# Kernel tuning notes

Measured on AMD Instinct MI355X. Metric: run time of the kernel, lower is better.

The kernel has to match this reference:

```python
import jax, jax.numpy as jnp
import numpy as np

EPS = 1e-6

def setup_inputs() -> dict:
    key = jax.random.key(0)
    ks = jax.random.split(key, 12)
    B, C, H, W = 2, 192, 192, 192
    f = lambda k, s, sc=1.0: jax.random.normal(k, s, dtype=jnp.float32) * sc
    d = {}
    d["x_l"] = f(ks[0], (B, C, H, W))
    d["x_r"] = f(ks[1], (B, C, H, W))
    d["ln_l_w"] = jnp.ones((C,), jnp.float32)
    d["ln_l_b"] = jnp.zeros((C,), jnp.float32)
    d["ln_r_w"] = jnp.ones((C,), jnp.float32)
    d["ln_r_b"] = jnp.zeros((C,), jnp.float32)
    s = C ** -0.5
    d["wq_l"] = f(ks[2], (C, C), s)   # 1x1 conv weights as [out,in]
    d["wq_r"] = f(ks[3], (C, C), s)
    d["wv_l"] = f(ks[4], (C, C), s)
    d["wv_r"] = f(ks[5], (C, C), s)
    d["mlp_w1"] = f(ks[6], (C // 24, C // 3), (C // 3) ** -0.5)
    d["mlp_w2"] = f(ks[7], (C * 2 // 3, C // 24), (C // 24) ** -0.5)
    d["scale_h"] = jnp.ones((1,), jnp.float32)
    d["scale_w"] = jnp.ones((1,), jnp.float32)
    # layer scales are zero-init in the module; use small random so output is nontrivial
    d["ls1"] = f(ks[8], (1, C, 1, 1), 0.1)
    d["ls2"] = f(ks[9], (1, C, 1, 1), 0.1)
    return d

def _ln2d(x, w, b):
    # LayerNorm over channel dim of NCHW
    mu = x.mean(1, keepdims=True)
    var = ((x - mu) ** 2).mean(1, keepdims=True)
    return (x - mu) * jax.lax.rsqrt(var + EPS) * w[None, :, None, None] + b[None, :, None, None]

def _pw(x, w):
    # 1x1 conv, no bias
    return jnp.einsum('bchw,oc->bohw', x, w)

def reference(x_l, x_r, ln_l_w, ln_l_b, ln_r_w, ln_r_b, wq_l, wq_r, wv_l, wv_r,
              mlp_w1, mlp_w2, scale_h, scale_w, ls1, ls2):
    q_l_h, q_l_w, q_l_c = jnp.split(_pw(_ln2d(x_l, ln_l_w, ln_l_b), wq_l), 3, axis=1)
    q_r_h, q_r_w, q_r_c = jnp.split(_pw(_ln2d(x_r, ln_r_w, ln_r_b), wq_r), 3, axis=1)
    v_l_h, v_l_w, v_l_c = jnp.split(_pw(x_l, wv_l), 3, axis=1)
    v_r_h, v_r_w, v_r_c = jnp.split(_pw(x_r, wv_r), 3, axis=1)

    # height axial attention: scores [b, w, h, h']
    attn_h = jnp.einsum('bchw,bcgw->bwhg', q_l_h, q_r_h) * scale_h[0]
    attn_h = jax.nn.softmax(attn_h, axis=-1)
    x_r2l_h = jnp.einsum('bwhg,bcgw->bchw', attn_h, v_r_h)           # [b,c,h,w]
    x_l2r_h = jnp.einsum('bwhg,bchw->bcgw', attn_h, v_l_h)           # attn^T @ v_l

    # width axial attention: scores [b, h, w, w'] (softmax applied separately per direction)
    attn_w = jnp.einsum('bchw,bchv->bhwv', q_l_w, q_r_w) * scale_w[0]
    a1 = jax.nn.softmax(attn_w, axis=-1)
    x_r2l_w = jnp.einsum('bhwv,bchv->bchw', a1, v_r_w)
    a2 = jax.nn.softmax(jnp.swapaxes(attn_w, -1, -2), axis=-1)       # [b,h,v,w]
    x_l2r_w = jnp.einsum('bhvw,bchw->bchv', a2, v_l_w)

    # channel SE branch: sum of the two channel queries, GAP, bottleneck MLP
    p = (q_l_c + q_r_c).mean(axis=(2, 3))                            # [b, c]
    h1 = jax.nn.relu(p @ mlp_w1.T)                                   # [b, c//8]
    a = jax.nn.softmax(h1 @ mlp_w2.T, axis=1)                        # softmax over 2c channels jointly
    attn_l_c, attn_r_c = jnp.split(a, 2, axis=1)
    x_r2l_c = attn_l_c[:, :, None, None] * v_l_c
    x_l2r_c = attn_r_c[:, :, None, None] * v_r_c

    x_r2l = jnp.concatenate([x_r2l_h, x_r2l_w, x_r2l_c], axis=1)
    x_l2r = jnp.concatenate([x_l2r_h, x_l2r_w, x_l2r_c], axis=1)
    out_l = x_r2l * ls1 + x_l
    out_r = x_l2r * ls2 + x_r
    return (out_l, out_r)
```

## Files before the change

kernel.cpp:

```cpp
#include <hip/hip_runtime.h>
#include <stdint.h>

#define NN 36864
#define PL 7077888
#define PL64 2359296
#define TOT 14155776

typedef unsigned short ushort_t;
typedef __attribute__((ext_vector_type(8))) __bf16 bf16x8;
typedef __attribute__((ext_vector_type(4))) float f32x4;
typedef __attribute__((ext_vector_type(4))) unsigned int u32x4;
typedef __attribute__((ext_vector_type(2))) unsigned int u32x2;

__device__ __forceinline__ ushort_t f2bf(float f) {
  unsigned int u = __builtin_bit_cast(unsigned int, f);
  u = (u + 0x7FFFu + ((u >> 16) & 1u)) >> 16;
  return (ushort_t)u;
}
__device__ __forceinline__ float bf2f(ushort_t h) {
  unsigned int u = ((unsigned int)h) << 16;
  return __builtin_bit_cast(float, u);
}
__device__ __forceinline__ bf16x8 lds8(const ushort_t* p) {
  return __builtin_bit_cast(bf16x8, *(const u32x4*)p);
}
__device__ __forceinline__ f32x4 mfma16(bf16x8 a, bf16x8 b, f32x4 c) {
  return __builtin_amdgcn_mfma_f32_16x16x32_bf16(a, b, c, 0, 0, 0);
}
__device__ __forceinline__ unsigned cvtpk(float lo, float hi) {
  unsigned r;
  asm("v_cvt_pk_bf16_f32 %0, %1, %2" : "=v"(r) : "v"(lo), "v"(hi));
  return r;
}

__global__ void k_prep(const float* __restrict__ wq, const float* __restrict__ wv,
                       const float* __restrict__ lnw, const float* __restrict__ lnb,
                       ushort_t* __restrict__ W, float* __restrict__ ab) {
  __shared__ float sa[3], sb[3];
  int r = blockIdx.x, t = threadIdx.x;
  if (r < 192) {
    float w  = wq[r*192 + t];
    float lw = lnw[t], lb = lnb[t];
    W[r*192 + t] = f2bf(w * lw);
    float av = w * lb, bv = -w * lw;
    #pragma unroll
    for (int off = 1; off < 64; off <<= 1) {
      av += __shfl_xor(av, off);
      bv += __shfl_xor(bv, off);
    }
    if ((t & 63) == 0) { sa[t >> 6] = av; sb[t >> 6] = bv; }
    __syncthreads();
    if (t == 0) { ab[r] = sa[0]+sa[1]+sa[2]; ab[192 + r] = sb[0]+sb[1]+sb[2]; }
  } else {
    W[r*192 + t] = f2bf(wv[(r-192)*192 + t]);
  }
}

__global__ __launch_bounds__(512, 6) void k_proj(
    const float* __restrict__ xl, const float* __restrict__ xr,
    const ushort_t* __restrict__ Wl, const ushort_t* __restrict__ Wr,
    const float* __restrict__ abl, const float* __restrict__ abr,
    ushort_t* __restrict__ qhTl, ushort_t* __restrict__ qhTr,
    ushort_t* __restrict__ qwTl, ushort_t* __restrict__ qwTr,
    ushort_t* __restrict__ Vl, ushort_t* __restrict__ Vr,
    float* __restrict__ gpart) {
  __shared__ union {
    ushort_t B[64*192];
    ushort_t T[64*72];
  } sm;
  __shared__ float spart[8][64], spart2[8][64];
  __shared__ float smu[64], srs[64];
  __shared__ float gsum[64];

  const int bx = blockIdx.x;
  const int side = bx & 1;
  const int r0 = bx >> 1;
  const int ws = r0 % 3, bh = r0 / 3;
  const int b = bh / 192, h = bh % 192;
  const int w0 = ws * 64;

  const float*    x  = side ? xr  : xl;
  const ushort_t* W  = side ? Wr  : Wl;
  const float*    ab = side ? abr : abl;
  ushort_t* qhT = side ? qhTr : qhTl;
  ushort_t* qwT = side ? qwTr : qwTl;
  ushort_t* V   = side ? Vr   : Vl;

  const int tid = threadIdx.x;
  const int wave = tid >> 6, lane = tid & 63, lr = lane & 15, lg = lane >> 4;

  if (tid < 64) gsum[tid] = 0.f;

  {
    const int kq = wave, n = lane;
    const float* xb = x + (size_t)b*PL + h*192 + w0 + n;
    float gv[24];
    #pragma unroll
    for (int s = 0; s < 6; ++s)
      #pragma unroll
      for (int j = 0; j < 4; ++j)
        gv[s*4 + j] = xb[(size_t)(s*32 + kq*4 + j)*NN];
    float sA = 0.f, sB = 0.f;
    char* Bb = (char*)sm.B;
    const int slot = 16*((kq >> 1) ^ ((n >> 1) & 3)) + 8*(kq & 1);
    #pragma unroll
    for (int s = 0; s < 6; ++s) {
      union { ushort_t us[4]; u32x2 v; } t2;
      #pragma unroll
      for (int j = 0; j < 4; ++j) {
        float g = gv[s*4 + j];
        t2.us[j] = f2bf(g);
        sA += g; sB += g*g;
      }
      *(u32x2*)(Bb + n*384 + s*64 + slot) = t2.v;
    }
    spart[kq][n] = sA; spart2[kq][n] = sB;
  }
  __syncthreads();

  if (tid < 64) {
    float s = 0.f, s2 = 0.f;
    #pragma unroll
    for (int q = 0; q < 8; ++q) { s += spart[q][tid]; s2 += spart2[q][tid]; }
    float mu = s * (1.f/192.f);
    float var = s2 * (1.f/192.f) - mu*mu;
    smu[tid] = mu;
    srs[tid] = rsqrtf(var + 1e-6f);
  }

  const ushort_t* wbase = W + (size_t)(48*wave + lr)*192 + lg*8;
  const char* Bb = (const char*)sm.B;
  const f32x4 fz = {0.f, 0.f, 0.f, 0.f};
  f32x4 acc[3][4];
  #pragma unroll
  for (int mf = 0; mf < 3; ++mf)
    #pragma unroll
    for (int nf = 0; nf < 4; ++nf) acc[mf][nf] = fz;

  #pragma unroll
  for (int ks = 0; ks < 6; ++ks) {
    bf16x8 bfr[4];
    #pragma unroll
    for (int nf = 0; nf < 4; ++nf) {
      int n_ = nf*16 + lr;
      bfr[nf] = lds8((const ushort_t*)(Bb + n_*384 + ks*64 + 16*(lg ^ ((n_ >> 1) & 3))));
    }
    bf16x8 afr[3];
    #pragma unroll
    for (int mf = 0; mf < 3; ++mf)
      afr[mf] = lds8(wbase + (size_t)mf*16*192 + ks*32);
    #pragma unroll
    for (int mf = 0; mf < 3; ++mf)
      #pragma unroll
      for (int nf = 0; nf < 4; ++nf)
        acc[mf][nf] = mfma16(afr[mf], bfr[nf], acc[mf][nf]);
  }
  __syncthreads();

  if (wave < 4) {
    float rst[4], mrs[4];
    #pragma unroll
    for (int nf = 0; nf < 4; ++nf) {
      int n_ = nf*16 + lr;
      float rs = srs[n_];
      rst[nf] = rs;
      mrs[nf] = smu[n_] * rs;
    }
    #pragma unroll
    for (int mf = 0; mf < 3; ++mf) {
      int m = 48*wave + 16*mf + 4*lg;
      #pragma unroll
      for (int i = 0; i < 4; ++i) {
        float a_ = ab[m + i], bb = ab[192 + m + i];
        #pragma unroll
        for (int nf = 0; nf < 4; ++nf)
          acc[mf][nf][i] = acc[mf][nf][i]*rst[nf] + bb*mrs[nf] + a_;
      }
    }
  }

  char* Tb = (char*)sm.T;
  if (wave < 4) {
    #pragma unroll
    for (int mf = 0; mf < 3; ++mf) {
      int base = 48*wave + 16*mf;
      if ((base >> 6) == 0) {
        #pragma unroll
        for (int nf = 0; nf < 4; ++nf) {
          u32x2 v = { cvtpk(acc[mf][nf][0], acc[mf][nf][1]),
                      cvtpk(acc[mf][nf][2], acc[mf][nf][3]) };
          *(u32x2*)(Tb + (nf*16 + lr)*144 + (base + 4*lg)*2) = v;
        }
      }
    }
  }
  __syncthreads();
  {
    int w = tid >> 3, c8 = tid & 7;
    u32x4 v = *(const u32x4*)(Tb + w*144 + c8*16);
    *(u32x4*)&qhT[(((size_t)b*192 + w0 + w)*192 + h)*64 + c8*8] = v;
  }
  __syncthreads();

  if (wave < 4) {
    #pragma unroll
    for (int mf = 0; mf < 3; ++mf) {
      int base = 48*wave + 16*mf;
      if ((base >> 6) == 1) {
        #pragma unroll
        for (int nf = 0; nf < 4; ++nf) {
          u32x2 v = { cvtpk(acc[mf][nf][0], acc[mf][nf][1]),
                      cvtpk(acc[mf][nf][2], acc[mf][nf][3]) };
          *(u32x2*)(Tb + (nf*16 + lr)*144 + (base - 64 + 4*lg)*2) = v;
        }
      }
    }
  }
  __syncthreads();
  {
    int w = tid >> 3, c8 = tid & 7;
    u32x4 v = *(const u32x4*)(Tb + w*144 + c8*16);
    *(u32x4*)&qwT[(((size_t)b*192 + h)*192 + w0 + w)*64 + c8*8] = v;
  }
  __syncthreads();

  #pragma unroll
  for (int ch = 0; ch < 3; ++ch) {
    if (wave >= 4) {
      #pragma unroll
      for (int mf = 0; mf < 3; ++mf) {
        int vc = 48*(wave - 4) + 16*mf;
        if ((vc >> 6) == ch) {
          int cc = vc - 64*ch + 4*lg;
          #pragma unroll
          for (int nf = 0; nf < 4; ++nf)
            #pragma unroll
            for (int i = 0; i < 4; ++i)
              *(ushort_t*)(Tb + (cc + i)*144 + (nf*16 + lr)*2) = f2bf(acc[mf][nf][i]);
        }
      }
    } else if (ch == 0) {
      #pragma unroll
      for (int mf = 0; mf < 3; ++mf) {
        int base = 48*wave + 16*mf;
        if ((base >> 6) == 2) {
          #pragma unroll
          for (int i = 0; i < 4; ++i) {
            float part = acc[mf][0][i] + acc[mf][1][i] + acc[mf][2][i] + acc[mf][3][i];
            #pragma unroll
            for (int off = 1; off < 16; off <<= 1) part += __shfl_xor(part, off);
            if (lr == 0) atomicAdd(&gsum[base - 128 + 4*lg + i], part);
          }
        }
      }
    }
    __syncthreads();
    {
      int cc = tid >> 3, w8 = tid & 7;
      u32x4 v = *(const u32x4*)(Tb + cc*144 + w8*16);
      *(u32x4*)&V[((size_t)b*192 + ch*64 + cc)*NN + h*192 + w0 + w8*8] = v;
    }
    if (ch == 0 && tid < 64)
      gpart[(((size_t)(side*2 + b)*192 + h)*3 + ws)*64 + tid] = gsum[tid];
    __syncthreads();
  }
}

__global__ void k_repack_v(const ushort_t* __restrict__ Vl, const ushort_t* __restrict__ Vr,
                           ushort_t* __restrict__ vhTl, ushort_t* __restrict__ vhTr) {
  __shared__ ushort_t Ls[64*72];
  const ushort_t* V = blockIdx.y ? Vr : Vl;
  ushort_t* out = blockIdx.y ? vhTr : vhTl;
  int bx = blockIdx.x;
  int b = bx / 576, rem = bx % 576;
  int c = rem / 9, tt = rem % 9;
  int h0 = (tt/3)*64, w0 = (tt%3)*64;
  int tid = threadIdx.x;
  #pragma unroll
  for (int i = 0; i < 2; ++i) {
    int idx = tid + 256*i;
    int hh = idx >> 3, wb = idx & 7;
    *(u32x4*)&Ls[hh*72 + wb*8] =
      *(const u32x4*)&V[(size_t)(b*192 + c)*NN + (h0+hh)*192 + w0 + wb*8];
  }
  __syncthreads();
  #pragma unroll
  for (int i = 0; i < 2; ++i) {
    int idx = tid + 256*i;
    int ww = idx >> 3, hb = idx & 7;
    union { ushort_t us[8]; u32x4 v; } tu;
    #pragma unroll
    for (int j = 0; j < 8; ++j) tu.us[j] = Ls[(hb*8+j)*72 + ww];
    *(u32x4*)&out[(size_t)(b*64 + c)*NN + (w0+ww)*192 + h0 + hb*8] = tu.v;
  }
}

__global__ __launch_bounds__(256, 2) void k_attn(
    const ushort_t* __restrict__ qhTl, const ushort_t* __restrict__ qhTr,
    const ushort_t* __restrict__ qwTl, const ushort_t* __restrict__ qwTr,
    const ushort_t* __restrict__ Vl,  const ushort_t* __restrict__ Vr,
    const ushort_t* __restrict__ vhTl, const ushort_t* __restrict__ vhTr,
    const float* __restrict__ sch, const float* __restrict__ scw,
    ushort_t* __restrict__ Oh1, ushort_t* __restrict__ Oh2,
    ushort_t* __restrict__ Ow1, ushort_t* __restrict__ Ow2) {
  __shared__ ushort_t Qsl[192*64];
  __shared__ ushort_t Qsr[192*64];
  __shared__ ushort_t Vs[64*192];
  __shared__ float md[192*2];

  const int tid = threadIdx.x;
  const int wave = tid >> 6, lane = tid & 63, lr = lane & 15, lg = lane >> 4;
  const int bx = blockIdx.x;
  const int mode = bx / 384;
  const int b = (bx % 384) / 192, s0 = bx % 192;
  const float scl = (mode ? scw : sch)[0];

  const ushort_t* ql = (mode ? qwTl : qhTl) + (size_t)(b*192 + s0)*12288;
  const ushort_t* qr = (mode ? qwTr : qhTr) + (size_t)(b*192 + s0)*12288;
  const ushort_t* vr = mode ? Vr + (size_t)(b*192 + 64)*NN + s0*192
                            : vhTr + (size_t)b*PL64 + s0*192;
  const ushort_t* vl = mode ? Vl + (size_t)(b*192 + 64)*NN + s0*192
                            : vhTl + (size_t)b*PL64 + s0*192;
  ushort_t* og1 = (mode ? Ow1 : Oh1) + (size_t)(b*192 + s0)*12288;
  ushort_t* og2 = (mode ? Ow2 : Oh2) + (size_t)(b*192 + s0)*12288;

  #pragma unroll
  for (int i = 0; i < 6; ++i) {
    int idx = tid + 256*i;
    int r = idx >> 3, sl = idx & 7;
    int dq = r*64 + ((sl ^ (r & 7)) << 3);
    *(u32x4*)&Qsl[dq] = *(const u32x4*)&ql[idx*8];
    *(u32x4*)&Qsr[dq] = *(const u32x4*)&qr[idx*8];
    int c = idx / 24, gs = idx % 24;
    *(u32x4*)&Vs[c*192 + ((gs ^ (c & 7)) << 3)] = *(const u32x4*)&vr[(size_t)c*NN + gs*8];
  }
  __syncthreads();

  const f32x4 fz = {0.f, 0.f, 0.f, 0.f};
  f32x4 acc[12][3];
  unsigned pk[3][12][2];

  auto qk = [&](bool swap) {
    const ushort_t* A  = swap ? Qsl : Qsr;
    const ushort_t* Bq = swap ? Qsr : Qsl;
    #pragma unroll
    for (int mf = 0; mf < 12; ++mf)
      #pragma unroll
      for (int nf = 0; nf < 3; ++nf) acc[mf][nf] = fz;
    __builtin_amdgcn_s_setprio(1);
    #pragma unroll
    for (int kh = 0; kh < 2; ++kh) {
      bf16x8 bq[3];
      #pragma unroll
      for (int nf = 0; nf < 3; ++nf) {
        int r = wave*48 + nf*16 + lr;
        bq[nf] = lds8(&Bq[r*64 + (((kh*4 + lg) ^ (r & 7)) << 3)]);
      }
      #pragma unroll
      for (int mf = 0; mf < 12; ++mf) {
        int r = mf*16 + lr;
        bf16x8 aq = lds8(&A[r*64 + (((kh*4 + lg) ^ (r & 7)) << 3)]);
        #pragma unroll
        for (int nf = 0; nf < 3; ++nf) acc[mf][nf] = mfma16(aq, bq[nf], acc[mf][nf]);
      }
    }
    __builtin_amdgcn_s_setprio(0);
  };

  auto smpack = [&](bool store_md) {
    #pragma unroll
    for (int nf = 0; nf < 3; ++nf) {
      float mx = -3.4e38f;
      #pragma unroll
      for (int mf = 0; mf < 12; ++mf)
        #pragma unroll
        for (int i = 0; i < 4; ++i) {
          float v = acc[mf][nf][i] * scl;
          acc[mf][nf][i] = v;
          mx = fmaxf(mx, v);
        }
      mx = fmaxf(mx, __shfl_xor(mx, 16));
      mx = fmaxf(mx, __shfl_xor(mx, 32));
      float den = 0.f;
      #pragma unroll
      for (int mf = 0; mf < 12; ++mf)
        #pragma unroll
        for (int i = 0; i < 4; ++i) {
          float e = __expf(acc[mf][nf][i] - mx);
          acc[mf][nf][i] = e;
          den += e;
        }
      den += __shfl_xor(den, 16);
      den += __shfl_xor(den, 32);
      float rd = 1.f / den;
      if (store_md && lg == 0) {
        int col = wave*48 + nf*16 + lr;
        md[col*2] = mx; md[col*2+1] = rd;
      }
      #pragma unroll
      for (int mf = 0; mf < 12; ++mf) {
        pk[nf][mf][0] = cvtpk(acc[mf][nf][0]*rd, acc[mf][nf][1]*rd);
        pk[nf][mf][1] = cvtpk(acc[mf][nf][2]*rd, acc[mf][nf][3]*rd);
      }
    }
  };

  auto pv = [&](unsigned obf[4][3][2]) {
    f32x4 o[4][3];
    #pragma unroll
    for (int mf = 0; mf < 4; ++mf)
      #pragma unroll
      for (int nf = 0; nf < 3; ++nf) o[mf][nf] = fz;
    const int sA = lr + 32*(lg & 1), sB = sA + 16;
    const bool hi = (lg >> 1) != 0;
    __builtin_amdgcn_s_setprio(1);
    #pragma unroll
    for (int ks = 0; ks < 6; ++ks) {
      bf16x8 av[4];
      #pragma unroll
      for (int mf = 0; mf < 4; ++mf) {
        int c = mf*16 + lr;
        av[mf] = lds8(&Vs[c*192 + (((4*ks + lg) ^ (c & 7)) << 3)]);
      }
      #pragma unroll
      for (int nf = 0; nf < 3; ++nf) {
        unsigned w0a = (unsigned)__shfl((int)pk[nf][2*ks  ][0], sA);
        unsigned w0b = (unsigned)__shfl((int)pk[nf][2*ks+1][0], sA);
        unsigned w1a = (unsigned)__shfl((int)pk[nf][2*ks  ][1], sA);
        unsigned w1b = (unsigned)__shfl((int)pk[nf][2*ks+1][1], sA);
        unsigned w2a = (unsigned)__shfl((int)pk[nf][2*ks  ][0], sB);
        unsigned w2b = (unsigned)__shfl((int)pk[nf][2*ks+1][0], sB);
        unsigned w3a = (unsigned)__shfl((int)pk[nf][2*ks  ][1], sB);
        unsigned w3b = (unsigned)__shfl((int)pk[nf][2*ks+1][1], sB);
        u32x4 wv = { hi ? w0b : w0a, hi ? w1b : w1a, hi ? w2b : w2a, hi ? w3b : w3a };
        bf16x8 bp = __builtin_bit_cast(bf16x8, wv);
        #pragma unroll
        for (int mf = 0; mf < 4; ++mf) o[mf][nf] = mfma16(av[mf], bp, o[mf][nf]);
      }
    }
    __builtin_amdgcn_s_setprio(0);
    #pragma unroll
    for (int mf = 0; mf < 4; ++mf)
      #pragma unroll
      for (int nf = 0; nf < 3; ++nf) {
        obf[mf][nf][0] = cvtpk(o[mf][nf][0], o[mf][nf][1]);
        obf[mf][nf][1] = cvtpk(o[mf][nf][2], o[mf][nf][3]);
      }
  };

  auto owrite = [&](unsigned obf[4][3][2]) {
    char* Ot = (char*)Qsl;
    #pragma unroll
    for (int mf = 0; mf < 4; ++mf)
      #pragma unroll
      for (int nf = 0; nf < 3; ++nf) {
        int col = wave*48 + nf*16 + lr;
        int byte = col*128 + ((mf*32 + lg*8) ^ ((col & 7) << 4));
        u32x2 v = { obf[mf][nf][0], obf[mf][nf][1] };
        *(u32x2*)(Ot + byte) = v;
      }
  };

  auto ostore = [&](ushort_t* og) {
    const char* Ot = (const char*)Qsl;
    #pragma unroll
    for (int it = 0; it < 6; ++it) {
      int id = tid + 256*it;
      int col = id >> 3, s = id & 7;
      int byte = col*128 + ((s*16) ^ ((col & 7) << 4));
      u32x4 v = *(const u32x4*)(Ot + byte);
      *(u32x4*)&og[(size_t)col*64 + s*8] = v;
    }
  };

  qk(false);
  smpack(true);
  unsigned o1bf[4][3][2];
  pv(o1bf);

  u32x4 vlr[6];
  #pragma unroll
  for (int i = 0; i < 6; ++i) {
    int idx = tid + 256*i;
    int c = idx / 24, gs = idx % 24;
    vlr[i] = *(const u32x4*)&vl[(size_t)c*NN + gs*8];
  }

  qk(true);
  __syncthreads();

  owrite(o1bf);
  #pragma unroll
  for (int i = 0; i < 6; ++i) {
    int idx = tid + 256*i;
    int c = idx / 24, gs = idx % 24;
    *(u32x4*)&Vs[c*192 + ((gs ^ (c & 7)) << 3)] = vlr[i];
  }

  if (mode == 0) {
    #pragma unroll
    for (int mf = 0; mf < 12; ++mf)
      #pragma unroll
      for (int i = 0; i < 4; ++i) {
        int row = mf*16 + lg*4 + i;
        float m_ = md[row*2], rd_ = md[row*2+1];
        #pragma unroll
        for (int nf = 0; nf < 3; ++nf)
          acc[mf][nf][i] = __expf(acc[mf][nf][i]*scl - m_) * rd_;
      }
    #pragma unroll
    for (int nf = 0; nf < 3; ++nf)
      #pragma unroll
      for (int mf = 0; mf < 12; ++mf) {
        pk[nf][mf][0] = cvtpk(acc[mf][nf][0], acc[mf][nf][1]);
        pk[nf][mf][1] = cvtpk(acc[mf][nf][2], acc[mf][nf][3]);
      }
  } else {
    smpack(false);
  }
  __syncthreads();

  ostore(og1);
  unsigned o2bf[4][3][2];
  pv(o2bf);
  __syncthreads();
  owrite(o2bf);
  __syncthreads();
  ostore(og2);
}

__global__ void k_se(const float* __restrict__ gpart, const float* __restrict__ w1,
                     const float* __restrict__ w2, float* __restrict__ sea) {
  __shared__ float psum[256];
  __shared__ float p[2][64];
  __shared__ float h1[2][8];
  __shared__ float lgt[2][128];
  __shared__ float mred[2], dred[2];
  int t = threadIdx.x;
  {
    int b = t >> 7, sideh = (t >> 6) & 1, c = t & 63;
    float s = 0.f;
    #pragma unroll 8
    for (int j = 0; j < 576; ++j)
      s += gpart[((size_t)(sideh*2 + b)*576 + j)*64 + c];
    psum[t] = s;
  }
  __syncthreads();
  if (t < 128) {
    int b = t >> 6, c = t & 63;
    p[b][c] = (psum[b*128 + c] + psum[b*128 + 64 + c]) * (1.f/36864.f);
  }
  __syncthreads();
  if (t < 16) {
    int bb = t >> 3, j = t & 7;
    float s = 0.f;
    for (int k = 0; k < 64; ++k) s += p[bb][k] * w1[j*64 + k];
    h1[bb][j] = fmaxf(s, 0.f);
  }
  __syncthreads();
  {
    int bb = t >> 7, o = t & 127;
    float s = 0.f;
    #pragma unroll
    for (int j = 0; j < 8; ++j) s += h1[bb][j] * w2[o*8 + j];
    lgt[bb][o] = s;
  }
  __syncthreads();
  if (t < 2) {
    float mx = -3.4e38f;
    for (int o = 0; o < 128; ++o) mx = fmaxf(mx, lgt[t][o]);
    float d = 0.f;
    for (int o = 0; o < 128; ++o) d += __expf(lgt[t][o] - mx);
    mred[t] = mx; dred[t] = d;
  }
  __syncthreads();
  {
    int bb = t >> 7, o = t & 127;
    sea[bb*128 + o] = __expf(lgt[bb][o] - mred[bb]) / dred[bb];
  }
}

__global__ __launch_bounds__(256, 4) void k_ep(
    const ushort_t* __restrict__ Oh1, const ushort_t* __restrict__ Oh2,
    const ushort_t* __restrict__ Ow1, const ushort_t* __restrict__ Ow2,
    const ushort_t* __restrict__ Vl, const ushort_t* __restrict__ Vr,
    const float* __restrict__ sea,
    const float* __restrict__ xl, const float* __restrict__ xr,
    const float* __restrict__ ls1, const float* __restrict__ ls2,
    float* __restrict__ out) {
  __shared__ ushort_t T[192*64];
  const int gid = blockIdx.x;
  const int h = gid % 192;
  const int b = (gid / 192) % 2;
  const int dir = gid / 384;
  const int tid = threadIdx.x;
  const float* xin = dir ? xr : xl;
  const float* ls  = dir ? ls2 : ls1;
  const ushort_t* Oh = dir ? Oh2 : Oh1;
  const ushort_t* Ow = dir ? Ow2 : Ow1;
  const ushort_t* Vv = dir ? Vr  : Vl;
  float* outp = out + (size_t)dir*TOT;

  const int c0 = (tid / 24) * 8, wseg = tid % 24, w0 = wseg * 8;
  const int Srd = (wseg & 7) << 4;

  auto flush = [&](int cbase) {
    if (tid < 192) {
      u32x4 r[8];
      #pragma unroll
      for (int j = 0; j < 8; ++j)
        r[j] = *(const u32x4*)((const char*)T + (w0 + j)*128 + ((c0*2) ^ Srd));
      #pragma unroll
      for (int k = 0; k < 8; ++k) {
        int c = cbase + c0 + k;
        float lsv = ls[c];
        size_t oo = (size_t)(b*192 + c)*NN + h*192 + w0;
        f32x4 xa = *(const f32x4*)&xin[oo];
        f32x4 xb2 = *(const f32x4*)&xin[oo + 4];
        f32x4 r0, r1;
        #pragma unroll
        for (int j = 0; j < 4; ++j) r0[j] = bf2f(((const ushort_t*)&r[j])[k])*lsv + xa[j];
        #pragma unroll
        for (int j = 0; j < 4; ++j) r1[j] = bf2f(((const ushort_t*)&r[4+j])[k])*lsv + xb2[j];
        *(f32x4*)&outp[oo] = r0;
        *(f32x4*)&outp[oo + 4] = r1;
      }
    }
  };

  {
    const ushort_t* ohb = Oh + ((size_t)b*192*192 + h)*64;
    #pragma unroll
    for (int it = 0; it < 6; ++it) {
      int id = tid + 256*it;
      int w = id >> 3, s = id & 7;
      u32x4 v = *(const u32x4*)&ohb[(size_t)w*12288 + s*8];
      *(u32x4*)((char*)T + w*128 + ((s*16) ^ (((w >> 3) & 7) << 4))) = v;
    }
  }
  __syncthreads();
  flush(0);
  __syncthreads();

  {
    const ushort_t* owb = Ow + ((size_t)b*192 + h)*12288;
    #pragma unroll
    for (int it = 0; it < 6; ++it) {
      int id = tid + 256*it;
      int w = id >> 3, s = id & 7;
      u32x4 v = *(const u32x4*)&owb[id*8];
      *(u32x4*)((char*)T + w*128 + ((s*16) ^ (((w >> 3) & 7) << 4))) = v;
    }
  }
  __syncthreads();
  flush(64);

  #pragma unroll
  for (int it = 0; it < 6; ++it) {
    int id = tid + 256*it;
    int cc = id / 24, ws = (id % 24) * 8;
    float lsv = ls[128 + cc] * sea[b*128 + dir*64 + cc];
    size_t oo = (size_t)(b*192 + 128 + cc)*NN + h*192 + ws;
    u32x4 sv = *(const u32x4*)&Vv[(size_t)(b*192 + 128 + cc)*NN + h*192 + ws];
    const ushort_t* sp = (const ushort_t*)&sv;
    f32x4 xa = *(const f32x4*)&xin[oo];
    f32x4 xb2 = *(const f32x4*)&xin[oo + 4];
    f32x4 r0, r1;
    #pragma unroll
    for (int j = 0; j < 4; ++j) r0[j] = bf2f(sp[j])*lsv + xa[j];
    #pragma unroll
    for (int j = 0; j < 4; ++j) r1[j] = bf2f(sp[4+j])*lsv + xb2[j];
    *(f32x4*)&outp[oo] = r0;
    *(f32x4*)&outp[oo + 4] = r1;
  }
}

extern "C" void kernel_launch(void* const* d_in, const int* in_sizes, int n_in,
                              void* d_out, int out_size, void* d_ws, size_t ws_size,
                              hipStream_t stream) {
  const float* x_l  = (const float*)d_in[0];
  const float* x_r  = (const float*)d_in[1];
  const float* lnlw = (const float*)d_in[2];
  const float* lnlb = (const float*)d_in[3];
  const float* lnrw = (const float*)d_in[4];
  const float* lnrb = (const float*)d_in[5];
  const float* wq_l = (const float*)d_in[6];
  const float* wq_r = (const float*)d_in[7];
  const float* wv_l = (const float*)d_in[8];
  const float* wv_r = (const float*)d_in[9];
  const float* w1   = (const float*)d_in[10];
  const float* w2   = (const float*)d_in[11];
  const float* sch  = (const float*)d_in[12];
  const float* scw  = (const float*)d_in[13];
  const float* ls1  = (const float*)d_in[14];
  const float* ls2  = (const float*)d_in[15];
  float* out = (float*)d_out;

  char* ws = (char*)d_ws;
  size_t off = 0;
  auto alloc = [&](size_t bytes) {
    char* p = ws + off;
    off += (bytes + 255) & ~(size_t)255;
    return p;
  };
  ushort_t* Vl   = (ushort_t*)alloc((size_t)2*192*NN*2);
  ushort_t* Vr   = (ushort_t*)alloc((size_t)2*192*NN*2);
  ushort_t* qhTl = (ushort_t*)alloc((size_t)2*64*NN*2);
  ushort_t* qhTr = (ushort_t*)alloc((size_t)2*64*NN*2);
  ushort_t* qwTl = (ushort_t*)alloc((size_t)2*64*NN*2);
  ushort_t* qwTr = (ushort_t*)alloc((size_t)2*64*NN*2);
  ushort_t* vhTl = (ushort_t*)alloc((size_t)2*64*NN*2);
  ushort_t* vhTr = (ushort_t*)alloc((size_t)2*64*NN*2);
  ushort_t* Oh1  = (ushort_t*)alloc((size_t)2*64*NN*2);
  ushort_t* Oh2  = (ushort_t*)alloc((size_t)2*64*NN*2);
  ushort_t* Ow1  = (ushort_t*)alloc((size_t)2*64*NN*2);
  ushort_t* Ow2  = (ushort_t*)alloc((size_t)2*64*NN*2);
  ushort_t* Wl   = (ushort_t*)alloc((size_t)384*192*2);
  ushort_t* Wr   = (ushort_t*)alloc((size_t)384*192*2);
  float* abl = (float*)alloc(384*4);
  float* abr = (float*)alloc(384*4);
  float* gpart = (float*)alloc((size_t)2*2*576*64*4);
  float* sea = (float*)alloc(2*128*4);
  (void)in_sizes; (void)n_in; (void)out_size; (void)ws_size;

  k_prep<<<384, 192, 0, stream>>>(wq_l, wv_l, lnlw, lnlb, Wl, abl);
  k_prep<<<384, 192, 0, stream>>>(wq_r, wv_r, lnrw, lnrb, Wr, abr);
  k_proj<<<2304, 512, 0, stream>>>(x_l, x_r, Wl, Wr, abl, abr,
                                   qhTl, qhTr, qwTl, qwTr, Vl, Vr, gpart);
  k_repack_v<<<dim3(1152, 2), 256, 0, stream>>>(Vl, Vr, vhTl, vhTr);
  k_attn<<<768, 256, 0, stream>>>(qhTl, qhTr, qwTl, qwTr, Vl, Vr, vhTl, vhTr,
                                  sch, scw, Oh1, Oh2, Ow1, Ow2);
  k_se<<<1, 256, 0, stream>>>(gpart, w1, w2, sea);
  k_ep<<<768, 256, 0, stream>>>(Oh1, Oh2, Ow1, Ow2, Vl, Vr, sea,
                                x_l, x_r, ls1, ls2, out);
}
```

Measured before the change: 262.8 us.

## Halve k_proj pixel tile to 32 columns with 256-thread blocks

The projection kernel now handles 32 pixels per block with 4 waves instead of 64 pixels with 8 waves. Each wave computes 96 output rows by 32 pixels, and the grid doubles to 4608 blocks. The shared-memory LDS atomic reduction for the channel-branch pooling is replaced by direct per-block partial writes, so the SE kernel sums twice as many partials. The aim is smaller LDS and register footprint per block for better occupancy and latency hiding. In exchange, the bf16 weight matrix is fetched from global memory twice as often overall, and each weight fragment is reused across fewer pixels.

```diff
diff --git a/kernel.cpp b/kernel.cpp
--- a/kernel.cpp
+++ b/kernel.cpp
@@ -56,7 +56,7 @@
   }
 }
 
-__global__ __launch_bounds__(512, 6) void k_proj(
+__global__ __launch_bounds__(256, 6) void k_proj(
     const float* __restrict__ xl, const float* __restrict__ xr,
     const ushort_t* __restrict__ Wl, const ushort_t* __restrict__ Wr,
     const float* __restrict__ abl, const float* __restrict__ abr,
@@ -65,19 +65,19 @@
     ushort_t* __restrict__ Vl, ushort_t* __restrict__ Vr,
     float* __restrict__ gpart) {
   __shared__ union {
-    ushort_t B[64*192];
-    ushort_t T[64*72];
+    ushort_t B[32*192];
+    ushort_t T[32*72];
+    ushort_t Tv[64*40];
   } sm;
-  __shared__ float spart[8][64], spart2[8][64];
-  __shared__ float smu[64], srs[64];
-  __shared__ float gsum[64];
+  __shared__ float spart[8][32], spart2[8][32];
+  __shared__ float smu[32], srs[32];
 
   const int bx = blockIdx.x;
   const int side = bx & 1;
   const int r0 = bx >> 1;
-  const int ws = r0 % 3, bh = r0 / 3;
+  const int wq = r0 % 6, bh = r0 / 6;
   const int b = bh / 192, h = bh % 192;
-  const int w0 = ws * 64;
+  const int w0 = wq * 32;
 
   const float*    x  = side ? xr  : xl;
   const ushort_t* W  = side ? Wr  : Wl;
@@ -89,36 +89,38 @@
   const int tid = threadIdx.x;
   const int wave = tid >> 6, lane = tid & 63, lr = lane & 15, lg = lane >> 4;
 
-  if (tid < 64) gsum[tid] = 0.f;
-
   {
-    const int kq = wave, n = lane;
+    const int kg = tid >> 5, n = tid & 31;
     const float* xb = x + (size_t)b*PL + h*192 + w0 + n;
-    float gv[24];
-    #pragma unroll
-    for (int s = 0; s < 6; ++s)
-      #pragma unroll
-      for (int j = 0; j < 4; ++j)
-        gv[s*4 + j] = xb[(size_t)(s*32 + kq*4 + j)*NN];
+    char* Bb = (char*)sm.B;
+    const int slot = 16*((kg >> 1) ^ ((n >> 1) & 3)) + 8*(kg & 1);
     float sA = 0.f, sB = 0.f;
-    char* Bb = (char*)sm.B;
-    const int slot = 16*((kq >> 1) ^ ((n >> 1) & 3)) + 8*(kq & 1);
-    #pragma unroll
-    for (int s = 0; s < 6; ++s) {
-      union { ushort_t us[4]; u32x2 v; } t2;
-      #pragma unroll
-      for (int j = 0; j < 4; ++j) {
-        float g = gv[s*4 + j];
-        t2.us[j] = f2bf(g);
-        sA += g; sB += g*g;
-      }
-      *(u32x2*)(Bb + n*384 + s*64 + slot) = t2.v;
-    }
-    spart[kq][n] = sA; spart2[kq][n] = sB;
-  }
-  __syncthreads();
-
-  if (tid < 64) {
+    #pragma unroll
+    for (int half = 0; half < 2; ++half) {
+      float gv[12];
+      #pragma unroll
+      for (int s = 0; s < 3; ++s)
+        #pragma unroll
+        for (int j = 0; j < 4; ++j)
+          gv[s*4 + j] = xb[(size_t)((half*3 + s)*32 + kg*4 + j)*NN];
+      #pragma unroll
+      for (int s = 0; s < 3; ++s) {
+        int ss = half*3 + s;
+        union { ushort_t us[4]; u32x2 v; } t2;
+        #pragma unroll
+        for (int j = 0; j < 4; ++j) {
+          float g = gv[s*4 + j];
+          t2.us[j] = f2bf(g);
+          sA += g; sB += g*g;
+        }
+        *(u32x2*)(Bb + n*384 + ss*64 + slot) = t2.v;
+      }
+    }
+    spart[kg][n] = sA; spart2[kg][n] = sB;
+  }
+  __syncthreads();
+
+  if (tid < 32) {
     float s = 0.f, s2 = 0.f;
     #pragma unroll
     for (int q = 0; q < 8; ++q) { s += spart[q][tid]; s2 += spart2[q][tid]; }
@@ -128,69 +130,64 @@
     srs[tid] = rsqrtf(var + 1e-6f);
   }
 
-  const ushort_t* wbase = W + (size_t)(48*wave + lr)*192 + lg*8;
+  const ushort_t* wbase = W + (size_t)(96*wave + lr)*192 + lg*8;
   const char* Bb = (const char*)sm.B;
   const f32x4 fz = {0.f, 0.f, 0.f, 0.f};
-  f32x4 acc[3][4];
-  #pragma unroll
-  for (int mf = 0; mf < 3; ++mf)
-    #pragma unroll
-    for (int nf = 0; nf < 4; ++nf) acc[mf][nf] = fz;
+  f32x4 acc[6][2];
+  #pragma unroll
+  for (int mf = 0; mf < 6; ++mf)
+    #pragma unroll
+    for (int nf = 0; nf < 2; ++nf) acc[mf][nf] = fz;
 
   #pragma unroll
   for (int ks = 0; ks < 6; ++ks) {
-    bf16x8 bfr[4];
-    #pragma unroll
-    for (int nf = 0; nf < 4; ++nf) {
+    bf16x8 bfr[2];
+    #pragma unroll
+    for (int nf = 0; nf < 2; ++nf) {
       int n_ = nf*16 + lr;
       bfr[nf] = lds8((const ushort_t*)(Bb + n_*384 + ks*64 + 16*(lg ^ ((n_ >> 1) & 3))));
     }
-    bf16x8 afr[3];
-    #pragma unroll
-    for (int mf = 0; mf < 3; ++mf)
-      afr[mf] = lds8(wbase + (size_t)mf*16*192 + ks*32);
-    #pragma unroll
-    for (int mf = 0; mf < 3; ++mf)
-      #pragma unroll
-      for (int nf = 0; nf < 4; ++nf)
-        acc[mf][nf] = mfma16(afr[mf], bfr[nf], acc[mf][nf]);
-  }
-  __syncthreads();
-
-  if (wave < 4) {
-    float rst[4], mrs[4];
-    #pragma unroll
-    for (int nf = 0; nf < 4; ++nf) {
+    #pragma unroll
+    for (int mf = 0; mf < 6; ++mf) {
+      bf16x8 afr = lds8(wbase + (size_t)mf*16*192 + ks*32);
+      #pragma unroll
+      for (int nf = 0; nf < 2; ++nf)
+        acc[mf][nf] = mfma16(afr, bfr[nf], acc[mf][nf]);
+    }
+  }
+  __syncthreads();
+
+  if (wave < 2) {
+    float rst[2], mrs[2];
+    #pragma unroll
+    for (int nf = 0; nf < 2; ++nf) {
       int n_ = nf*16 + lr;
       float rs = srs[n_];
       rst[nf] = rs;
       mrs[nf] = smu[n_] * rs;
     }
     #pragma unroll
-    for (int mf = 0; mf < 3; ++mf) {
-      int m = 48*wave + 16*mf + 4*lg;
+    for (int mf = 0; mf < 6; ++mf) {
+      int m = 96*wave + 16*mf + 4*lg;
       #pragma unroll
       for (int i = 0; i < 4; ++i) {
         float a_ = ab[m + i], bb = ab[192 + m + i];
         #pragma unroll
-        for (int nf = 0; nf < 4; ++nf)
+        for (int nf = 0; nf < 2; ++nf)
           acc[mf][nf][i] = acc[mf][nf][i]*rst[nf] + bb*mrs[nf] + a_;
       }
     }
   }
 
   char* Tb = (char*)sm.T;
-  if (wave < 4) {
-    #pragma unroll
-    for (int mf = 0; mf < 3; ++mf) {
-      int base = 48*wave + 16*mf;
-      if ((base >> 6) == 0) {
-        #pragma unroll
-        for (int nf = 0; nf < 4; ++nf) {
-          u32x2 v = { cvtpk(acc[mf][nf][0], acc[mf][nf][1]),
-                      cvtpk(acc[mf][nf][2], acc[mf][nf][3]) };
-          *(u32x2*)(Tb + (nf*16 + lr)*144 + (base + 4*lg)*2) = v;
-        }
+  if (wave == 0) {
+    #pragma unroll
+    for (int mf = 0; mf < 4; ++mf) {
+      #pragma unroll
+      for (int nf = 0; nf < 2; ++nf) {
+        u32x2 v = { cvtpk(acc[mf][nf][0], acc[mf][nf][1]),
+                    cvtpk(acc[mf][nf][2], acc[mf][nf][3]) };
+        *(u32x2*)(Tb + (nf*16 + lr)*144 + (16*mf + 4*lg)*2) = v;
       }
     }
   }
@@ -202,13 +199,13 @@
   }
   __syncthreads();
 
-  if (wave < 4) {
-    #pragma unroll
-    for (int mf = 0; mf < 3; ++mf) {
-      int base = 48*wave + 16*mf;
+  if (wave < 2) {
+    #pragma unroll
+    for (int mf = 0; mf < 6; ++mf) {
+      int base = 96*wave + 16*mf;
       if ((base >> 6) == 1) {
         #pragma unroll
-        for (int nf = 0; nf < 4; ++nf) {
+        for (int nf = 0; nf < 2; ++nf) {
           u32x2 v = { cvtpk(acc[mf][nf][0], acc[mf][nf][1]),
                       cvtpk(acc[mf][nf][2], acc[mf][nf][3]) };
           *(u32x2*)(Tb + (nf*16 + lr)*144 + (base - 64 + 4*lg)*2) = v;
@@ -224,44 +221,44 @@
   }
   __syncthreads();
 
+  if (wave == 1) {
+    #pragma unroll
+    for (int mf = 2; mf < 6; ++mf) {
+      #pragma unroll
+      for (int i = 0; i < 4; ++i) {
+        float part = acc[mf][0][i] + acc[mf][1][i];
+        #pragma unroll
+        for (int off = 1; off < 16; off <<= 1) part += __shfl_xor(part, off);
+        if (lr == 0) {
+          int row = 16*(mf - 2) + 4*lg + i;
+          gpart[(((size_t)(side*2 + b)*192 + h)*6 + wq)*64 + row] = part;
+        }
+      }
+    }
+  }
+
   #pragma unroll
   for (int ch = 0; ch < 3; ++ch) {
-    if (wave >= 4) {
-      #pragma unroll
-      for (int mf = 0; mf < 3; ++mf) {
-        int vc = 48*(wave - 4) + 16*mf;
+    if (wave >= 2) {
+      #pragma unroll
+      for (int mf = 0; mf < 6; ++mf) {
+        int vc = 96*(wave - 2) + 16*mf;
         if ((vc >> 6) == ch) {
           int cc = vc - 64*ch + 4*lg;
           #pragma unroll
-          for (int nf = 0; nf < 4; ++nf)
+          for (int nf = 0; nf < 2; ++nf)
             #pragma unroll
             for (int i = 0; i < 4; ++i)
-              *(ushort_t*)(Tb + (cc + i)*144 + (nf*16 + lr)*2) = f2bf(acc[mf][nf][i]);
-        }
-      }
-    } else if (ch == 0) {
-      #pragma unroll
-      for (int mf = 0; mf < 3; ++mf) {
-        int base = 48*wave + 16*mf;
-        if ((base >> 6) == 2) {
-          #pragma unroll
-          for (int i = 0; i < 4; ++i) {
-            float part = acc[mf][0][i] + acc[mf][1][i] + acc[mf][2][i] + acc[mf][3][i];
-            #pragma unroll
-            for (int off = 1; off < 16; off <<= 1) part += __shfl_xor(part, off);
-            if (lr == 0) atomicAdd(&gsum[base - 128 + 4*lg + i], part);
-          }
+              *(ushort_t*)(Tb + (cc + i)*80 + (nf*16 + lr)*2) = f2bf(acc[mf][nf][i]);
         }
       }
     }
     __syncthreads();
     {
-      int cc = tid >> 3, w8 = tid & 7;
-      u32x4 v = *(const u32x4*)(Tb + cc*144 + w8*16);
+      int cc = tid >> 2, w8 = tid & 3;
+      u32x4 v = *(const u32x4*)(Tb + cc*80 + w8*16);
       *(u32x4*)&V[((size_t)b*192 + ch*64 + cc)*NN + h*192 + w0 + w8*8] = v;
     }
-    if (ch == 0 && tid < 64)
-      gpart[(((size_t)(side*2 + b)*192 + h)*3 + ws)*64 + tid] = gsum[tid];
     __syncthreads();
   }
 }
@@ -541,8 +538,8 @@
     int b = t >> 7, sideh = (t >> 6) & 1, c = t & 63;
     float s = 0.f;
     #pragma unroll 8
-    for (int j = 0; j < 576; ++j)
-      s += gpart[((size_t)(sideh*2 + b)*576 + j)*64 + c];
+    for (int j = 0; j < 1152; ++j)
+      s += gpart[((size_t)(sideh*2 + b)*1152 + j)*64 + c];
     psum[t] = s;
   }
   __syncthreads();
@@ -719,13 +716,13 @@
   ushort_t* Wr   = (ushort_t*)alloc((size_t)384*192*2);
   float* abl = (float*)alloc(384*4);
   float* abr = (float*)alloc(384*4);
-  float* gpart = (float*)alloc((size_t)2*2*576*64*4);
+  float* gpart = (float*)alloc((size_t)2*2*1152*64*4);
   float* sea = (float*)alloc(2*128*4);
   (void)in_sizes; (void)n_in; (void)out_size; (void)ws_size;
 
   k_prep<<<384, 192, 0, stream>>>(wq_l, wv_l, lnlw, lnlb, Wl, abl);
   k_prep<<<384, 192, 0, stream>>>(wq_r, wv_r, lnrw, lnrb, Wr, abr);
-  k_proj<<<2304, 512, 0, stream>>>(x_l, x_r, Wl, Wr, abl, abr,
+  k_proj<<<4608, 256, 0, stream>>>(x_l, x_r, Wl, Wr, abl, abr,
                                    qhTl, qhTr, qwTl, qwTr, Vl, Vr, gpart);
   k_repack_v<<<dim3(1152, 2), 256, 0, stream>>>(Vl, Vr, vhTl, vhTr);
   k_attn<<<768, 256, 0, stream>>>(qhTl, qhTr, qwTl, qwTr, Vl, Vr, vhTl, vhTr,
```

After: 364.3 us. 38.6% more time.
